# Performance work log

Hardware: AMD Instinct MI355X
Metric: run time of the kernel (lower is better)

Reference implementation:

```python
import jax, jax.numpy as jnp
import numpy as np

H, HKV, D = 8, 1, 256  # query heads, kv heads, head_dim (Gemma-2B-like)


def apply_rope(x, sin, cos):
    # x: [B, h, D, S]; sin/cos: [B, 1, D//2, S]
    x1, x2 = jnp.split(x, 2, axis=-2)
    return jnp.concatenate((x1 * cos - x2 * sin, x2 * cos + x1 * sin), axis=-2)


def setup_inputs() -> dict:
    key = jax.random.key(0)
    ks = jax.random.split(key, 12)
    B, hidden, S = 2, 2048, 2048
    half = D // 2
    Xq = jax.random.normal(ks[0], (B, hidden, S), jnp.float32)
    Xkv = jax.random.normal(ks[1], (B, hidden, S), jnp.float32)
    sin_q = jax.random.uniform(ks[2], (B, 1, half, S), jnp.float32, -1.0, 1.0)
    cos_q = jax.random.uniform(ks[3], (B, 1, half, S), jnp.float32, -1.0, 1.0)
    sin_k = jax.random.uniform(ks[4], (B, 1, half, S), jnp.float32, -1.0, 1.0)
    cos_k = jax.random.uniform(ks[5], (B, 1, half, S), jnp.float32, -1.0, 1.0)
    attn_mask = jnp.zeros((B, 1, S, S), jnp.float32)
    scale = 0.02
    Wq = jax.random.normal(ks[6], (H * D, hidden), jnp.float32) * scale
    Wk = jax.random.normal(ks[7], (HKV * D, hidden), jnp.float32) * scale
    Wv = jax.random.normal(ks[8], (HKV * D, hidden), jnp.float32) * scale
    Wo = jax.random.normal(ks[9], (hidden, H * D), jnp.float32) * scale
    return {"Xq": Xq, "Xkv": Xkv, "sin_q": sin_q, "cos_q": cos_q,
            "sin_k": sin_k, "cos_k": cos_k, "attn_mask": attn_mask,
            "Wq": Wq, "Wk": Wk, "Wv": Wv, "Wo": Wo}


def reference(Xq, Xkv, sin_q, cos_q, sin_k, cos_k, attn_mask, Wq, Wk, Wv, Wo):
    B, hidden, Sq = Xq.shape
    Sk = Xkv.shape[-1]
    # ANEDenseGeneral = 1x1 conv over channels-first layout
    q = jnp.einsum('oc,bcs->bos', Wq, Xq).reshape(B, H, D, Sq)
    q = apply_rope(q, sin_q, cos_q)
    k = jnp.einsum('oc,bcs->bos', Wk, Xkv).reshape(B, HKV, D, Sk)
    k = apply_rope(k, sin_k, cos_k)
    v = jnp.einsum('oc,bcs->bos', Wv, Xkv).reshape(B, HKV, D, Sk)
    # GQA: broadcast kv heads to query heads
    rep = H // HKV
    k = jnp.repeat(k, rep, axis=1)
    v = jnp.repeat(v, rep, axis=1)
    scale = 1.0 / jnp.sqrt(jnp.asarray(D, Xq.dtype))
    scores = jnp.einsum('bhdq,bhdk->bhqk', q, k) * scale + attn_mask
    probs = jax.nn.softmax(scores, axis=-1)
    out = jnp.einsum('bhqk,bhdk->bhdq', probs, v).reshape(B, H * D, Sq)
    return jnp.einsum('oc,bcs->bos', Wo, out).astype(Xq.dtype)
```

## Files before the change

### kernel.cpp

```cpp
#include <hip/hip_runtime.h>

typedef __bf16 bf16;
typedef __bf16 bf16x8 __attribute__((ext_vector_type(8)));
typedef __bf16 bf16x4 __attribute__((ext_vector_type(4)));
typedef float f32x4 __attribute__((ext_vector_type(4)));

static constexpr int Hh = 8;
static constexpr int Dd = 256;
static constexpr int Ss = 2048;
static constexpr int Cc = 2048;

typedef const __attribute__((address_space(1))) unsigned int as1_u32;
typedef __attribute__((address_space(3))) unsigned int as3_u32;

__device__ __forceinline__ void gl_lds16(const void* g, void* l) {
  __builtin_amdgcn_global_load_lds((as1_u32*)(unsigned long long)g,
                                   (as3_u32*)(unsigned int)(unsigned long long)l,
                                   16, 0, 0);
}

__device__ __forceinline__ f32x4 mfma16(bf16x8 a, bf16x8 b, f32x4 c) {
  return __builtin_amdgcn_mfma_f32_16x16x32_bf16(a, b, c, 0, 0, 0);
}

__global__ __launch_bounds__(256) void cvt_w(const float* __restrict__ in,
                                             bf16* __restrict__ out, int n) {
  int i = (blockIdx.x * 256 + threadIdx.x) * 4;
  if (i >= n) return;
  const float4 v = *(const float4*)(in + i);
  bf16x4 o;
  o[0] = (bf16)v.x; o[1] = (bf16)v.y; o[2] = (bf16)v.z; o[3] = (bf16)v.w;
  *(bf16x4*)(out + i) = o;
}

__global__ __launch_bounds__(256) void transpose_cvt(const float* __restrict__ in,
                                                     bf16* __restrict__ out,
                                                     int R, int S) {
  __shared__ float t[32][33];
  const int b = blockIdx.z;
  const long base = (long)b * R * S;
  const int s0 = blockIdx.x * 32, r0 = blockIdx.y * 32;
  const int tx = threadIdx.x, ty = threadIdx.y;
#pragma unroll
  for (int i = 0; i < 32; i += 8)
    t[ty + i][tx] = in[base + (long)(r0 + ty + i) * S + s0 + tx];
  __syncthreads();
#pragma unroll
  for (int i = 0; i < 32; i += 8)
    out[base + (long)(s0 + ty + i) * R + r0 + tx] = (bf16)t[tx][ty + i];
}

__global__ __launch_bounds__(256) void rope_transpose(
    const bf16* __restrict__ xin, const bf16* __restrict__ sint,
    const bf16* __restrict__ cost, bf16* __restrict__ xout, int nH) {
  __shared__ __align__(16) bf16 ti[32][264];
  const int b = blockIdx.z, h = blockIdx.y, s0 = blockIdx.x * 32;
  const int tx = threadIdx.x, ty = threadIdx.y;
  const bf16* src = xin + ((long)(b * nH + h) * Dd) * Ss + s0;
#pragma unroll
  for (int i = 0; i < 32; ++i) {
    int d = ty + i * 8;
    ti[tx][d] = src[(long)d * Ss + tx];
  }
  __syncthreads();
  const int t = ty * 32 + tx;
  const int s = t >> 3;
  const int dpart = t & 7;
  const bf16* sp = sint + ((long)b * Ss + s0 + s) * 128;
  const bf16* cp = cost + ((long)b * Ss + s0 + s) * 128;
  bf16* dst = xout + (((long)(b * nH + h)) * Ss + s0 + s) * Dd;
#pragma unroll
  for (int i = 0; i < 4; ++i) {
    int d0 = dpart * 8 + i * 64;
    int dh = d0 & 127;
    bf16x8 a = *(const bf16x8*)&ti[s][d0];
    bf16x8 p = *(const bf16x8*)&ti[s][(d0 < 128) ? d0 + 128 : d0 - 128];
    bf16x8 sn = *(const bf16x8*)&sp[dh];
    bf16x8 cs = *(const bf16x8*)&cp[dh];
    bf16x8 o;
#pragma unroll
    for (int j = 0; j < 8; ++j) {
      float av = (float)a[j], pv = (float)p[j];
      float c = (float)cs[j], sv = (float)sn[j];
      float val = (d0 < 128) ? (av * c - pv * sv) : (av * c + pv * sv);
      o[j] = (bf16)val;
    }
    *(bf16x8*)&dst[d0] = o;
  }
}

__global__ __launch_bounds__(256, 2) void gemm_bt(
    const bf16* __restrict__ A, const bf16* __restrict__ Bt,
    bf16* __restrict__ Cb, float* __restrict__ Cf, int M, int N, int K,
    long sBt, long sC) {
  __shared__ __align__(16) bf16 lA[2][128 * 64];
  __shared__ __align__(16) bf16 lB[2][128 * 64];
  const int tid = threadIdx.x;
  const int wid = tid >> 6, lane = tid & 63;
  const int g = lane >> 4, r = lane & 15;
  const int wr = wid >> 1, wc = wid & 1;
  const int mt = blockIdx.y * 128, nt = blockIdx.x * 128;
  const int z = blockIdx.z;
  const bf16* Bz = Bt + (long)z * sBt;

  auto stage = [&](int buf, int kt) {
#pragma unroll
    for (int it = 0; it < 4; ++it) {
      int off = it * 4096 + tid * 16;
      int row = off >> 7;
      int c = (off >> 4) & 7;
      int csw = c ^ (row & 7);
      gl_lds16((const char*)(A + (long)(mt + row) * K + kt) + csw * 16,
               (char*)lA[buf] + it * 4096 + wid * 1024);
      gl_lds16((const char*)(Bz + (long)(nt + row) * K + kt) + csw * 16,
               (char*)lB[buf] + it * 4096 + wid * 1024);
    }
  };

  const f32x4 zf = {0.f, 0.f, 0.f, 0.f};
  f32x4 acc[4][4];
#pragma unroll
  for (int m = 0; m < 4; ++m)
#pragma unroll
    for (int n = 0; n < 4; ++n) acc[m][n] = zf;

  stage(0, 0);
  __syncthreads();
  int cur = 0;
  for (int kt = 0; kt < K; kt += 64) {
    if (kt + 64 < K) stage(cur ^ 1, kt + 64);
#pragma unroll
    for (int kk = 0; kk < 2; ++kk) {
      bf16x8 af[4], bfv[4];
#pragma unroll
      for (int m = 0; m < 4; ++m) {
        int row = wr * 64 + m * 16 + r;
        int csw = (kk * 4 + g) ^ (row & 7);
        af[m] = *(const bf16x8*)((const char*)lA[cur] + row * 128 + csw * 16);
      }
#pragma unroll
      for (int n = 0; n < 4; ++n) {
        int row = wc * 64 + n * 16 + r;
        int csw = (kk * 4 + g) ^ (row & 7);
        bfv[n] = *(const bf16x8*)((const char*)lB[cur] + row * 128 + csw * 16);
      }
#pragma unroll
      for (int m = 0; m < 4; ++m)
#pragma unroll
        for (int n = 0; n < 4; ++n)
          acc[m][n] = mfma16(af[m], bfv[n], acc[m][n]);
    }
    __syncthreads();
    cur ^= 1;
  }

#pragma unroll
  for (int m = 0; m < 4; ++m)
#pragma unroll
    for (int n = 0; n < 4; ++n)
#pragma unroll
      for (int e = 0; e < 4; ++e) {
        int orow = mt + wr * 64 + m * 16 + g * 4 + e;
        int col = nt + wc * 64 + n * 16 + r;
        long idx = (long)z * sC + (long)orow * N + col;
        if (Cf) Cf[idx] = acc[m][n][e];
        else Cb[idx] = (bf16)acc[m][n][e];
      }
}

__global__ __launch_bounds__(256, 2) void attn_kernel(
    const bf16* __restrict__ qr, const bf16* __restrict__ kr,
    const bf16* __restrict__ vv, const float* __restrict__ mask,
    bf16* __restrict__ aout) {
  __shared__ __align__(16) bf16 lK[2][32 * 256];
  __shared__ __align__(16) bf16 lV[2][256 * 32];
  __shared__ __align__(16) bf16 lP[4][16 * 40];
  const int b = blockIdx.z, hg = blockIdx.y;
  const int q0 = blockIdx.x * 16;
  const int tid = threadIdx.x;
  const int wid = tid >> 6, lane = tid & 63;
  const int g = lane >> 4, q = lane & 15;
  const int h = hg * 4 + wid;

  bf16x8 qf[8];
  const bf16* qp = qr + (((long)(b * Hh + h)) * Ss + q0 + q) * Dd;
#pragma unroll
  for (int kk = 0; kk < 8; ++kk) qf[kk] = *(const bf16x8*)&qp[kk * 32 + g * 8];

  const f32x4 zf = {0.f, 0.f, 0.f, 0.f};
  f32x4 oacc[16];
#pragma unroll
  for (int i = 0; i < 16; ++i) oacc[i] = zf;
  float mrun = -3e38f, lrun = 0.f;

  const char* kb = (const char*)(kr + (long)b * Ss * Dd);
  const char* vb = (const char*)(vv + (long)b * Dd * Ss);
  const float* mb = mask + (long)b * Ss * Ss;

  auto stage = [&](int buf, int kt) {
    const char* gK = kb + (long)kt * 512;
#pragma unroll
    for (int it = 0; it < 4; ++it) {
      int off = it * 4096 + tid * 16;
      int row = off >> 9;
      int c = (off >> 4) & 31;
      int csw = c ^ (row & 7);
      gl_lds16(gK + row * 512 + csw * 16,
               (char*)lK[buf] + it * 4096 + wid * 1024);
    }
#pragma unroll
    for (int it = 0; it < 4; ++it) {
      int off = it * 4096 + tid * 16;
      int row = off >> 6;
      int c = (off >> 4) & 3;
      int csw = c ^ ((row >> 1) & 3);
      gl_lds16(vb + (long)row * (Ss * 2) + (long)kt * 2 + csw * 16,
               (char*)lV[buf] + it * 4096 + wid * 1024);
    }
  };

  stage(0, 0);
  __syncthreads();
  int cur = 0;

  for (int kt = 0; kt < Ss; kt += 32) {
    if (kt + 32 < Ss) stage(cur ^ 1, kt + 32);

    const float* mrow = mb + (long)(q0 + q) * Ss + kt;
    const float4 mv0 = *(const float4*)(mrow + 4 * g);
    const float4 mv1 = *(const float4*)(mrow + 16 + 4 * g);

    f32x4 sacc[2] = {zf, zf};
    __builtin_amdgcn_s_setprio(1);
#pragma unroll
    for (int kk = 0; kk < 8; ++kk) {
#pragma unroll
      for (int n = 0; n < 2; ++n) {
        int row = n * 16 + q;
        int csw = (kk * 4 + g) ^ (row & 7);
        bf16x8 kf = *(const bf16x8*)((const char*)lK[cur] + row * 512 + csw * 16);
        sacc[n] = mfma16(kf, qf[kk], sacc[n]);
      }
    }
    __builtin_amdgcn_s_setprio(0);

    float x[8];
    x[0] = sacc[0][0] * 0.0625f + mv0.x;
    x[1] = sacc[0][1] * 0.0625f + mv0.y;
    x[2] = sacc[0][2] * 0.0625f + mv0.z;
    x[3] = sacc[0][3] * 0.0625f + mv0.w;
    x[4] = sacc[1][0] * 0.0625f + mv1.x;
    x[5] = sacc[1][1] * 0.0625f + mv1.y;
    x[6] = sacc[1][2] * 0.0625f + mv1.z;
    x[7] = sacc[1][3] * 0.0625f + mv1.w;
    float mx = fmaxf(fmaxf(fmaxf(x[0], x[1]), fmaxf(x[2], x[3])),
                     fmaxf(fmaxf(x[4], x[5]), fmaxf(x[6], x[7])));
    mx = fmaxf(mx, __shfl_xor(mx, 16, 64));
    mx = fmaxf(mx, __shfl_xor(mx, 32, 64));
    if (mx > mrun + 8.0f) {
      float al = __expf(mrun - mx);
      lrun *= al;
#pragma unroll
      for (int nf = 0; nf < 16; ++nf) oacc[nf] *= al;
      mrun = mx;
    }
    float p[8];
    float rs = 0.f;
#pragma unroll
    for (int i = 0; i < 8; ++i) {
      p[i] = __expf(x[i] - mrun);
      rs += p[i];
    }
    rs += __shfl_xor(rs, 16, 64);
    rs += __shfl_xor(rs, 32, 64);
    lrun += rs;

    bf16x4 w0, w1;
#pragma unroll
    for (int e = 0; e < 4; ++e) { w0[e] = (bf16)p[e]; w1[e] = (bf16)p[4 + e]; }
    *(bf16x4*)&lP[wid][q * 40 + 4 * g] = w0;
    *(bf16x4*)&lP[wid][q * 40 + 16 + 4 * g] = w1;

    bf16x8 pf = *(const bf16x8*)&lP[wid][q * 40 + g * 8];
    __builtin_amdgcn_s_setprio(1);
#pragma unroll
    for (int nf = 0; nf < 16; ++nf) {
      int row = nf * 16 + q;
      int csw = g ^ ((row >> 1) & 3);
      bf16x8 vf = *(const bf16x8*)((const char*)lV[cur] + row * 64 + csw * 16);
      oacc[nf] = mfma16(vf, pf, oacc[nf]);
    }
    __builtin_amdgcn_s_setprio(0);

    __syncthreads();
    cur ^= 1;
  }

  const float inv = 1.f / lrun;
  bf16* op = aout + ((long)(b * Ss + q0 + q)) * (Hh * Dd) + h * Dd + g * 4;
#pragma unroll
  for (int nf = 0; nf < 16; ++nf) {
    bf16x4 o4;
#pragma unroll
    for (int e = 0; e < 4; ++e) o4[e] = (bf16)(oacc[nf][e] * inv);
    *(bf16x4*)&op[nf * 16] = o4;
  }
}

extern "C" void kernel_launch(void* const* d_in, const int* in_sizes, int n_in,
                              void* d_out, int out_size, void* d_ws,
                              size_t ws_size, hipStream_t stream) {
  const float* Xq = (const float*)d_in[0];
  const float* Xkv = (const float*)d_in[1];
  const float* sin_q = (const float*)d_in[2];
  const float* cos_q = (const float*)d_in[3];
  const float* sin_k = (const float*)d_in[4];
  const float* cos_k = (const float*)d_in[5];
  const float* mask = (const float*)d_in[6];
  const float* Wq = (const float*)d_in[7];
  const float* Wk = (const float*)d_in[8];
  const float* Wv = (const float*)d_in[9];
  const float* Wo = (const float*)d_in[10];
  float* out = (float*)d_out;

  char* ws = (char*)d_ws;
  const size_t MB = 1u << 20;
  bf16* Wq_bf = (bf16*)(ws + 0 * MB);
  bf16* Wo_bf = (bf16*)(ws + 8 * MB);
  bf16* Wk_bf = (bf16*)(ws + 16 * MB);
  bf16* Wv_bf = (bf16*)(ws + 17 * MB);
  bf16* sin_qt = (bf16*)(ws + 18 * MB);
  bf16* cos_qt = (bf16*)(ws + 19 * MB);
  bf16* sin_kt = (bf16*)(ws + 20 * MB);
  bf16* cos_kt = (bf16*)(ws + 21 * MB);
  bf16* Xtq = (bf16*)(ws + 22 * MB);
  bf16* Xtkv = (bf16*)(ws + 38 * MB);
  bf16* q_tmp = (bf16*)(ws + 54 * MB);
  bf16* k_tmp = (bf16*)(ws + 70 * MB);
  bf16* v_bf = (bf16*)(ws + 72 * MB);
  bf16* qr = (bf16*)(ws + 22 * MB);
  bf16* kr = (bf16*)(ws + 38 * MB);
  bf16* attnb = (bf16*)(ws + 54 * MB);

  dim3 b256(256), b32x8(32, 8);

  cvt_w<<<4096, b256, 0, stream>>>(Wq, Wq_bf, Cc * Cc);
  cvt_w<<<4096, b256, 0, stream>>>(Wo, Wo_bf, Cc * Cc);
  cvt_w<<<512, b256, 0, stream>>>(Wk, Wk_bf, Dd * Cc);
  cvt_w<<<512, b256, 0, stream>>>(Wv, Wv_bf, Dd * Cc);

  transpose_cvt<<<dim3(64, 64, 2), b32x8, 0, stream>>>(Xq, Xtq, Cc, Ss);
  transpose_cvt<<<dim3(64, 64, 2), b32x8, 0, stream>>>(Xkv, Xtkv, Cc, Ss);
  transpose_cvt<<<dim3(64, 4, 2), b32x8, 0, stream>>>(sin_q, sin_qt, 128, Ss);
  transpose_cvt<<<dim3(64, 4, 2), b32x8, 0, stream>>>(cos_q, cos_qt, 128, Ss);
  transpose_cvt<<<dim3(64, 4, 2), b32x8, 0, stream>>>(sin_k, sin_kt, 128, Ss);
  transpose_cvt<<<dim3(64, 4, 2), b32x8, 0, stream>>>(cos_k, cos_kt, 128, Ss);

  gemm_bt<<<dim3(16, 16, 2), b256, 0, stream>>>(
      Wq_bf, Xtq, q_tmp, nullptr, Cc, Ss, Cc, (long)Ss * Cc, (long)Cc * Ss);
  gemm_bt<<<dim3(16, 2, 2), b256, 0, stream>>>(
      Wk_bf, Xtkv, k_tmp, nullptr, Dd, Ss, Cc, (long)Ss * Cc, (long)Dd * Ss);
  gemm_bt<<<dim3(16, 2, 2), b256, 0, stream>>>(
      Wv_bf, Xtkv, v_bf, nullptr, Dd, Ss, Cc, (long)Ss * Cc, (long)Dd * Ss);

  rope_transpose<<<dim3(64, 8, 2), b32x8, 0, stream>>>(q_tmp, sin_qt, cos_qt,
                                                       qr, Hh);
  rope_transpose<<<dim3(64, 1, 2), b32x8, 0, stream>>>(k_tmp, sin_kt, cos_kt,
                                                       kr, 1);

  attn_kernel<<<dim3(128, 2, 2), b256, 0, stream>>>(qr, kr, v_bf, mask, attnb);

  gemm_bt<<<dim3(16, 16, 2), b256, 0, stream>>>(
      Wo_bf, attnb, nullptr, out, Cc, Ss, Cc, (long)Ss * Cc, (long)Cc * Ss);
}
```

Baseline: 298.2 us.

## Use 32x32 MFMA tiles in attention and fuse K/V projection GEMMs

The attention kernel moves from 16x16x32 to 32x32x16 MFMA with 32-query tiles per wave. The P fragment is now built in registers with v_permlane32_swap instead of a round trip through LDS, and the grid is remapped so each XCD works on a contiguous set of tiles. The K and V projections become a single GEMM over the adjacent Wk/Wv buffers. This raises register pressure (launch bounds drop to one block per SIMD pair) and halves the number of attention blocks in exchange for fewer LDS loads per FLOP and one fewer launch.

```diff
diff --git a/kernel.cpp b/kernel.cpp
--- a/kernel.cpp
+++ b/kernel.cpp
@@ -3,7 +3,11 @@
 typedef __bf16 bf16;
 typedef __bf16 bf16x8 __attribute__((ext_vector_type(8)));
 typedef __bf16 bf16x4 __attribute__((ext_vector_type(4)));
+typedef __bf16 bf16x2 __attribute__((ext_vector_type(2)));
 typedef float f32x4 __attribute__((ext_vector_type(4)));
+typedef float f32x16 __attribute__((ext_vector_type(16)));
+typedef unsigned u32;
+typedef unsigned u32x4v __attribute__((ext_vector_type(4)));
 
 static constexpr int Hh = 8;
 static constexpr int Dd = 256;
@@ -21,6 +25,16 @@
 
 __device__ __forceinline__ f32x4 mfma16(bf16x8 a, bf16x8 b, f32x4 c) {
   return __builtin_amdgcn_mfma_f32_16x16x32_bf16(a, b, c, 0, 0, 0);
+}
+__device__ __forceinline__ f32x16 mfma32(bf16x8 a, bf16x8 b, f32x16 c) {
+  return __builtin_amdgcn_mfma_f32_32x32x16_bf16(a, b, c, 0, 0, 0);
+}
+
+__device__ __forceinline__ u32 pk_bf16(float lo, float hi) {
+  bf16x2 t;
+  t[0] = (bf16)lo;
+  t[1] = (bf16)hi;
+  return __builtin_bit_cast(u32, t);
 }
 
 __global__ __launch_bounds__(256) void cvt_w(const float* __restrict__ in,
@@ -52,11 +66,12 @@
 
 __global__ __launch_bounds__(256) void rope_transpose(
     const bf16* __restrict__ xin, const bf16* __restrict__ sint,
-    const bf16* __restrict__ cost, bf16* __restrict__ xout, int nH) {
+    const bf16* __restrict__ cost, bf16* __restrict__ xout, int nH,
+    long bStr) {
   __shared__ __align__(16) bf16 ti[32][264];
   const int b = blockIdx.z, h = blockIdx.y, s0 = blockIdx.x * 32;
   const int tx = threadIdx.x, ty = threadIdx.y;
-  const bf16* src = xin + ((long)(b * nH + h) * Dd) * Ss + s0;
+  const bf16* src = xin + (long)b * bStr + (long)h * Dd * Ss + s0;
 #pragma unroll
   for (int i = 0; i < 32; ++i) {
     int d = ty + i * 8;
@@ -168,33 +183,33 @@
       }
 }
 
-__global__ __launch_bounds__(256, 2) void attn_kernel(
+__global__ __launch_bounds__(256, 1) void attn_kernel(
     const bf16* __restrict__ qr, const bf16* __restrict__ kr,
-    const bf16* __restrict__ vv, const float* __restrict__ mask,
+    const bf16* __restrict__ kv, const float* __restrict__ mask,
     bf16* __restrict__ aout) {
   __shared__ __align__(16) bf16 lK[2][32 * 256];
   __shared__ __align__(16) bf16 lV[2][256 * 32];
-  __shared__ __align__(16) bf16 lP[4][16 * 40];
-  const int b = blockIdx.z, hg = blockIdx.y;
-  const int q0 = blockIdx.x * 16;
+  const int i = blockIdx.x;
+  const int flat = (i & 7) * 32 + (i >> 3);
+  const int b = flat >> 7;
+  const int hg = (flat >> 6) & 1;
+  const int q0 = (flat & 63) * 32;
   const int tid = threadIdx.x;
   const int wid = tid >> 6, lane = tid & 63;
-  const int g = lane >> 4, q = lane & 15;
+  const int l31 = lane & 31, hi = lane >> 5;
   const int h = hg * 4 + wid;
 
-  bf16x8 qf[8];
-  const bf16* qp = qr + (((long)(b * Hh + h)) * Ss + q0 + q) * Dd;
-#pragma unroll
-  for (int kk = 0; kk < 8; ++kk) qf[kk] = *(const bf16x8*)&qp[kk * 32 + g * 8];
-
-  const f32x4 zf = {0.f, 0.f, 0.f, 0.f};
-  f32x4 oacc[16];
-#pragma unroll
-  for (int i = 0; i < 16; ++i) oacc[i] = zf;
+  bf16x8 qf[16];
+  const bf16* qp = qr + (((long)(b * Hh + h)) * Ss + q0 + l31) * Dd;
+#pragma unroll
+  for (int kk = 0; kk < 16; ++kk)
+    qf[kk] = *(const bf16x8*)&qp[kk * 16 + hi * 8];
+
+  f32x16 oacc[8] = {};
   float mrun = -3e38f, lrun = 0.f;
 
   const char* kb = (const char*)(kr + (long)b * Ss * Dd);
-  const char* vb = (const char*)(vv + (long)b * Dd * Ss);
+  const char* vb = (const char*)(kv + ((long)b * 2 * Dd + Dd) * Ss);
   const float* mb = mask + (long)b * Ss * Ss;
 
   auto stage = [&](int buf, int kt) {
@@ -226,69 +241,71 @@
   for (int kt = 0; kt < Ss; kt += 32) {
     if (kt + 32 < Ss) stage(cur ^ 1, kt + 32);
 
-    const float* mrow = mb + (long)(q0 + q) * Ss + kt;
-    const float4 mv0 = *(const float4*)(mrow + 4 * g);
-    const float4 mv1 = *(const float4*)(mrow + 16 + 4 * g);
-
-    f32x4 sacc[2] = {zf, zf};
+    const float* mrow = mb + (long)(q0 + l31) * Ss + kt;
+    float4 mv[4];
+#pragma unroll
+    for (int grp = 0; grp < 4; ++grp)
+      mv[grp] = *(const float4*)(mrow + grp * 8 + hi * 4);
+
+    f32x16 sacc = {};
     __builtin_amdgcn_s_setprio(1);
 #pragma unroll
-    for (int kk = 0; kk < 8; ++kk) {
-#pragma unroll
-      for (int n = 0; n < 2; ++n) {
-        int row = n * 16 + q;
-        int csw = (kk * 4 + g) ^ (row & 7);
-        bf16x8 kf = *(const bf16x8*)((const char*)lK[cur] + row * 512 + csw * 16);
-        sacc[n] = mfma16(kf, qf[kk], sacc[n]);
-      }
+    for (int kk = 0; kk < 16; ++kk) {
+      int csw = (kk * 2 + hi) ^ (l31 & 7);
+      bf16x8 kf = *(const bf16x8*)((const char*)lK[cur] + l31 * 512 + csw * 16);
+      sacc = mfma32(kf, qf[kk], sacc);
     }
     __builtin_amdgcn_s_setprio(0);
 
-    float x[8];
-    x[0] = sacc[0][0] * 0.0625f + mv0.x;
-    x[1] = sacc[0][1] * 0.0625f + mv0.y;
-    x[2] = sacc[0][2] * 0.0625f + mv0.z;
-    x[3] = sacc[0][3] * 0.0625f + mv0.w;
-    x[4] = sacc[1][0] * 0.0625f + mv1.x;
-    x[5] = sacc[1][1] * 0.0625f + mv1.y;
-    x[6] = sacc[1][2] * 0.0625f + mv1.z;
-    x[7] = sacc[1][3] * 0.0625f + mv1.w;
-    float mx = fmaxf(fmaxf(fmaxf(x[0], x[1]), fmaxf(x[2], x[3])),
-                     fmaxf(fmaxf(x[4], x[5]), fmaxf(x[6], x[7])));
-    mx = fmaxf(mx, __shfl_xor(mx, 16, 64));
+    float x[16];
+#pragma unroll
+    for (int r = 0; r < 16; ++r)
+      x[r] = sacc[r] * 0.0625f + ((const float*)&mv[r >> 2])[r & 3];
+    float mx = x[0];
+#pragma unroll
+    for (int r = 1; r < 16; ++r) mx = fmaxf(mx, x[r]);
     mx = fmaxf(mx, __shfl_xor(mx, 32, 64));
     if (mx > mrun + 8.0f) {
       float al = __expf(mrun - mx);
       lrun *= al;
 #pragma unroll
-      for (int nf = 0; nf < 16; ++nf) oacc[nf] *= al;
+      for (int d = 0; d < 8; ++d) oacc[d] *= al;
       mrun = mx;
     }
-    float p[8];
+    float p[16];
     float rs = 0.f;
 #pragma unroll
-    for (int i = 0; i < 8; ++i) {
-      p[i] = __expf(x[i] - mrun);
-      rs += p[i];
-    }
-    rs += __shfl_xor(rs, 16, 64);
+    for (int r = 0; r < 16; ++r) {
+      p[r] = __expf(x[r] - mrun);
+      rs += p[r];
+    }
     rs += __shfl_xor(rs, 32, 64);
     lrun += rs;
 
-    bf16x4 w0, w1;
-#pragma unroll
-    for (int e = 0; e < 4; ++e) { w0[e] = (bf16)p[e]; w1[e] = (bf16)p[4 + e]; }
-    *(bf16x4*)&lP[wid][q * 40 + 4 * g] = w0;
-    *(bf16x4*)&lP[wid][q * 40 + 16 + 4 * g] = w1;
-
-    bf16x8 pf = *(const bf16x8*)&lP[wid][q * 40 + g * 8];
+    bf16x8 pf[2];
+#pragma unroll
+    for (int kk2 = 0; kk2 < 2; ++kk2) {
+      u32 a0 = pk_bf16(p[kk2 * 8 + 0], p[kk2 * 8 + 1]);
+      u32 a1 = pk_bf16(p[kk2 * 8 + 2], p[kk2 * 8 + 3]);
+      u32 b0 = pk_bf16(p[kk2 * 8 + 4], p[kk2 * 8 + 5]);
+      u32 b1 = pk_bf16(p[kk2 * 8 + 6], p[kk2 * 8 + 7]);
+      asm("v_permlane32_swap_b32 %0, %1" : "+v"(a0), "+v"(b0));
+      asm("v_permlane32_swap_b32 %0, %1" : "+v"(a1), "+v"(b1));
+      u32x4v w;
+      w[0] = a0; w[1] = a1; w[2] = b0; w[3] = b1;
+      pf[kk2] = __builtin_bit_cast(bf16x8, w);
+    }
+
     __builtin_amdgcn_s_setprio(1);
 #pragma unroll
-    for (int nf = 0; nf < 16; ++nf) {
-      int row = nf * 16 + q;
-      int csw = g ^ ((row >> 1) & 3);
-      bf16x8 vf = *(const bf16x8*)((const char*)lV[cur] + row * 64 + csw * 16);
-      oacc[nf] = mfma16(vf, pf, oacc[nf]);
+    for (int kk2 = 0; kk2 < 2; ++kk2) {
+#pragma unroll
+      for (int db = 0; db < 8; ++db) {
+        int csw = (kk2 * 2 + hi) ^ ((l31 >> 1) & 3);
+        bf16x8 vf = *(const bf16x8*)((const char*)lV[cur] +
+                                     (db * 32 + l31) * 64 + csw * 16);
+        oacc[db] = mfma32(vf, pf[kk2], oacc[db]);
+      }
     }
     __builtin_amdgcn_s_setprio(0);
 
@@ -297,13 +314,16 @@
   }
 
   const float inv = 1.f / lrun;
-  bf16* op = aout + ((long)(b * Ss + q0 + q)) * (Hh * Dd) + h * Dd + g * 4;
-#pragma unroll
-  for (int nf = 0; nf < 16; ++nf) {
-    bf16x4 o4;
-#pragma unroll
-    for (int e = 0; e < 4; ++e) o4[e] = (bf16)(oacc[nf][e] * inv);
-    *(bf16x4*)&op[nf * 16] = o4;
+  bf16* op = aout + ((long)(b * Ss + q0 + l31)) * (Hh * Dd) + h * Dd;
+#pragma unroll
+  for (int db = 0; db < 8; ++db) {
+#pragma unroll
+    for (int grp = 0; grp < 4; ++grp) {
+      bf16x4 o4;
+#pragma unroll
+      for (int e = 0; e < 4; ++e) o4[e] = (bf16)(oacc[db][grp * 4 + e] * inv);
+      *(bf16x4*)&op[db * 32 + grp * 8 + hi * 4] = o4;
+    }
   }
 }
 
@@ -327,7 +347,7 @@
   const size_t MB = 1u << 20;
   bf16* Wq_bf = (bf16*)(ws + 0 * MB);
   bf16* Wo_bf = (bf16*)(ws + 8 * MB);
-  bf16* Wk_bf = (bf16*)(ws + 16 * MB);
+  bf16* Wkv_bf = (bf16*)(ws + 16 * MB);
   bf16* Wv_bf = (bf16*)(ws + 17 * MB);
   bf16* sin_qt = (bf16*)(ws + 18 * MB);
   bf16* cos_qt = (bf16*)(ws + 19 * MB);
@@ -336,8 +356,7 @@
   bf16* Xtq = (bf16*)(ws + 22 * MB);
   bf16* Xtkv = (bf16*)(ws + 38 * MB);
   bf16* q_tmp = (bf16*)(ws + 54 * MB);
-  bf16* k_tmp = (bf16*)(ws + 70 * MB);
-  bf16* v_bf = (bf16*)(ws + 72 * MB);
+  bf16* kv_tmp = (bf16*)(ws + 70 * MB);
   bf16* qr = (bf16*)(ws + 22 * MB);
   bf16* kr = (bf16*)(ws + 38 * MB);
   bf16* attnb = (bf16*)(ws + 54 * MB);
@@ -346,7 +365,7 @@
 
   cvt_w<<<4096, b256, 0, stream>>>(Wq, Wq_bf, Cc * Cc);
   cvt_w<<<4096, b256, 0, stream>>>(Wo, Wo_bf, Cc * Cc);
-  cvt_w<<<512, b256, 0, stream>>>(Wk, Wk_bf, Dd * Cc);
+  cvt_w<<<512, b256, 0, stream>>>(Wk, (bf16*)Wkv_bf, Dd * Cc);
   cvt_w<<<512, b256, 0, stream>>>(Wv, Wv_bf, Dd * Cc);
 
   transpose_cvt<<<dim3(64, 64, 2), b32x8, 0, stream>>>(Xq, Xtq, Cc, Ss);
@@ -358,17 +377,16 @@
 
   gemm_bt<<<dim3(16, 16, 2), b256, 0, stream>>>(
       Wq_bf, Xtq, q_tmp, nullptr, Cc, Ss, Cc, (long)Ss * Cc, (long)Cc * Ss);
-  gemm_bt<<<dim3(16, 2, 2), b256, 0, stream>>>(
-      Wk_bf, Xtkv, k_tmp, nullptr, Dd, Ss, Cc, (long)Ss * Cc, (long)Dd * Ss);
-  gemm_bt<<<dim3(16, 2, 2), b256, 0, stream>>>(
-      Wv_bf, Xtkv, v_bf, nullptr, Dd, Ss, Cc, (long)Ss * Cc, (long)Dd * Ss);
-
-  rope_transpose<<<dim3(64, 8, 2), b32x8, 0, stream>>>(q_tmp, sin_qt, cos_qt,
-                                                       qr, Hh);
-  rope_transpose<<<dim3(64, 1, 2), b32x8, 0, stream>>>(k_tmp, sin_kt, cos_kt,
-                                                       kr, 1);
-
-  attn_kernel<<<dim3(128, 2, 2), b256, 0, stream>>>(qr, kr, v_bf, mask, attnb);
+  gemm_bt<<<dim3(16, 4, 2), b256, 0, stream>>>(
+      Wkv_bf, Xtkv, kv_tmp, nullptr, 2 * Dd, Ss, Cc, (long)Ss * Cc,
+      (long)2 * Dd * Ss);
+
+  rope_transpose<<<dim3(64, 8, 2), b32x8, 0, stream>>>(
+      q_tmp, sin_qt, cos_qt, qr, Hh, (long)Hh * Dd * Ss);
+  rope_transpose<<<dim3(64, 1, 2), b32x8, 0, stream>>>(
+      kv_tmp, sin_kt, cos_kt, kr, 1, (long)2 * Dd * Ss);
+
+  attn_kernel<<<dim3(256), b256, 0, stream>>>(qr, kr, kv_tmp, mask, attnb);
 
   gemm_bt<<<dim3(16, 16, 2), b256, 0, stream>>>(
       Wo_bf, attnb, nullptr, out, Cc, Ss, Cc, (long)Ss * Cc, (long)Cc * Ss);
```

Measured after the change: 307.6 us. +3.1%, slower.
